# Performance work log

Hardware: AMD Instinct MI355X
Metric: run time of the kernel (lower is better)

Reference implementation:

```python
import jax, jax.numpy as jnp
import numpy as np

B, IN_DIM, D, C = 16384, 1024, 256, 100


def setup_inputs() -> dict:
    key = jax.random.key(0)
    k1, k2, k3, k4 = jax.random.split(key, 4)
    x = jax.random.normal(k1, (B, IN_DIM), dtype=jnp.float32)
    W = jax.random.normal(k2, (IN_DIM, D), dtype=jnp.float32) * (1.0 / np.sqrt(IN_DIM))
    b = jax.random.normal(k3, (D,), dtype=jnp.float32) * 0.01
    P = jax.random.normal(k4, (C, D), dtype=jnp.float32)  # class prototypes [C, D]
    return {"x": x, "W": W, "b": b, "P": P}


def reference(x, W, b, P):
    # Encoder: Z = x @ W + b  -> [B, D]
    Z = x @ W + b
    d = Z.shape[-1]
    # MSE(r, p) = mean((r - p)^2) = (|r|^2 - 2 r.p + |p|^2) / D
    # Computed via expansion to avoid the [B, C, D] broadcast intermediate.
    sq = (
        jnp.sum(Z * Z, axis=-1, keepdims=True)      # [B, 1]
        - 2.0 * (Z @ P.T)                            # [B, C]
        + jnp.sum(P * P, axis=-1)[None, :]           # [1, C]
    )
    return -sq / d  # [B, C]
```

## Files before the change

kernel.cpp:

```cpp
#include <hip/hip_runtime.h>

#define BATCH 16384
#define KDIM  1024
#define DDIM  256
#define CNUM  100
#define CPAD  112
#define RSTR  72

typedef __bf16 bf16x8 __attribute__((ext_vector_type(8)));
typedef float  floatx4 __attribute__((ext_vector_type(4)));

static __device__ __forceinline__ unsigned short f2b(float f) {
    return __builtin_bit_cast(unsigned short, (__bf16)f);
}

__global__ __launch_bounds__(256) void prep(const float* __restrict__ W,
                                            const float* __restrict__ P,
                                            unsigned short* __restrict__ Wt2,
                                            unsigned short* __restrict__ Pbf,
                                            float* __restrict__ pnorm2) {
    __shared__ float T[32][33];
    const int bid = blockIdx.x;
    if (bid < 256) {
        const int k0 = (bid & 31) * 32;
        const int n0 = (bid >> 5) * 32;
        const int j  = threadIdx.x & 31;
        const int i0 = threadIdx.x >> 5;
#pragma unroll
        for (int l = 0; l < 4; ++l) {
            int i = i0 + l * 8;
            T[i][j] = W[(k0 + i) * DDIM + n0 + j];
        }
        __syncthreads();
        if (threadIdx.x < 128) {
            const int l  = threadIdx.x & 63;
            const int fn = threadIdx.x >> 6;
            const int lm = l & 15, lq = l >> 4;
            bf16x8 v;
#pragma unroll
            for (int jj = 0; jj < 8; ++jj)
                v[jj] = (__bf16)T[lq * 8 + jj][fn * 16 + lm];
            const int nblk = (n0 >> 4) + fn;
            const int kblk = k0 >> 5;
            *(bf16x8*)&Wt2[(nblk * 32 + kblk) * 512 + l * 8] = v;
        }
    } else {
        const int wave = threadIdx.x >> 6;
        const int lane = threadIdx.x & 63;
        const int c = (bid - 256) * 4 + wave;
        float s = 0.f;
#pragma unroll
        for (int jj = 0; jj < 4; ++jj) {
            int d = jj * 64 + lane;
            float v = (c < CNUM) ? P[c * DDIM + d] : 0.f;
            Pbf[c * DDIM + d] = f2b(v);
            s += v * v;
        }
#pragma unroll
        for (int m = 1; m < 64; m <<= 1) s += __shfl_xor(s, m, 64);
        if (lane == 0) pnorm2[c] = s;
    }
}

#define CVT8(H, A_, B_)                                                        \
    H[0] = (__bf16)A_[0]; H[1] = (__bf16)A_[1];                                \
    H[2] = (__bf16)A_[2]; H[3] = (__bf16)A_[3];                                \
    H[4] = (__bf16)B_[0]; H[5] = (__bf16)B_[1];                                \
    H[6] = (__bf16)B_[2]; H[7] = (__bf16)B_[3];

#define MFMA_(A_, B_, C_) __builtin_amdgcn_mfma_f32_16x16x32_bf16(A_, B_, C_, 0, 0, 0)

#define GRAN(G, CUR)                                                           \
    {                                                                          \
        const unsigned short* As_c = U16 + (CUR) * 16384 + kh * 8192;          \
        _Pragma("unroll")                                                      \
        for (int kf = 0; kf < 2; ++kf) {                                       \
            const int sw = ((((G) & 1) * 8 + kf * 4 + lq) ^ lm) * 8;           \
            bf16x8 a0 = *(const bf16x8*)&As_c[lm * 128 + sw];                  \
            bf16x8 a1 = *(const bf16x8*)&As_c[(16 + lm) * 128 + sw];           \
            bf16x8 a2 = *(const bf16x8*)&As_c[(32 + lm) * 128 + sw];           \
            bf16x8 a3 = *(const bf16x8*)&As_c[(48 + lm) * 128 + sw];           \
            _Pragma("unroll")                                                  \
            for (int f = 0; f < 4; ++f) {                                      \
                acc[0][f] = MFMA_(a0, b[(G) & 1][kf * 4 + f], acc[0][f]);      \
                acc[1][f] = MFMA_(a1, b[(G) & 1][kf * 4 + f], acc[1][f]);      \
                acc[2][f] = MFMA_(a2, b[(G) & 1][kf * 4 + f], acc[2][f]);      \
                acc[3][f] = MFMA_(a3, b[(G) & 1][kf * 4 + f], acc[3][f]);      \
            }                                                                  \
        }                                                                      \
        if ((G) + 2 < 8) {                                                     \
            _Pragma("unroll")                                                  \
            for (int kf = 0; kf < 2; ++kf)                                     \
                _Pragma("unroll")                                              \
                for (int f = 0; f < 4; ++f)                                    \
                    b[(G) & 1][kf * 4 + f] = *(const bf16x8*)(gB +             \
                        f * 16384 + (((G) + 2) * 2 + kf) * 512);               \
        }                                                                      \
    }

#define PAIRSTEP(T, CUR, NXT)                                                  \
    {                                                                          \
        if ((T) < 3) {                                                         \
            bf16x8 h0, h1, h2, h3;                                             \
            CVT8(h0, p[0], p[1]) CVT8(h1, p[2], p[3])                          \
            CVT8(h2, p[4], p[5]) CVT8(h3, p[6], p[7])                          \
            *(bf16x8*)&U16[(NXT) * 16384 + ldsW0] = h0;                        \
            *(bf16x8*)&U16[(NXT) * 16384 + ldsW1] = h1;                        \
            *(bf16x8*)&U16[(NXT) * 16384 + 8192 + ldsW0] = h2;                 \
            *(bf16x8*)&U16[(NXT) * 16384 + 8192 + ldsW1] = h3;                 \
            if ((T) < 2) {                                                     \
                p[0] = *(const floatx4*)(gA + ((T) + 2) * 128);                \
                p[1] = *(const floatx4*)(gA + ((T) + 2) * 128 + 4);            \
                p[2] = *(const floatx4*)(gA + ((T) + 2) * 128 + 64);           \
                p[3] = *(const floatx4*)(gA + ((T) + 2) * 128 + 68);           \
                p[4] = *(const floatx4*)(gA + 512 + ((T) + 2) * 128);          \
                p[5] = *(const floatx4*)(gA + 512 + ((T) + 2) * 128 + 4);      \
                p[6] = *(const floatx4*)(gA + 512 + ((T) + 2) * 128 + 64);     \
                p[7] = *(const floatx4*)(gA + 512 + ((T) + 2) * 128 + 68);     \
            }                                                                  \
        }                                                                      \
        GRAN(2 * (T), CUR)                                                     \
        GRAN(2 * (T) + 1, CUR)                                                 \
        asm volatile("s_waitcnt lgkmcnt(0)\n\ts_barrier" ::: "memory");        \
    }

__global__ __launch_bounds__(512, 2) void fused_main(
    const float* __restrict__ x, const float* __restrict__ bias,
    const unsigned short* __restrict__ Wt2, const unsigned short* __restrict__ Pbf,
    const float* __restrict__ pnorm2, float* __restrict__ out)
{
    __shared__ __align__(16) float Ubuf[DDIM * RSTR];
    __shared__ float rn2[4][64];
    unsigned short* U16 = (unsigned short*)Ubuf;
    float* Rs = Ubuf;
    unsigned short* Zs = (unsigned short*)Ubuf;

    const int tid  = threadIdx.x;
    const int wave = tid >> 6;
    const int kh   = wave >> 2;
    const int wn   = wave & 3;
    const int lane = tid & 63;
    const int lm   = lane & 15;
    const int lq   = lane >> 4;
    const int r0   = blockIdx.x * 64;

    const int rowA = tid >> 3;
    const int kbA  = tid & 7;
    const float* gA = x + (size_t)(r0 + rowA) * KDIM + kbA * 8;
    const int ldsW0 = rowA * 128 + ((kbA ^ (rowA & 15)) * 8);
    const int ldsW1 = rowA * 128 + (((kbA + 8) ^ (rowA & 15)) * 8);

    const unsigned short* gB = Wt2 + wn * 65536 + kh * 8192 + lane * 8;

    floatx4 acc[4][4];
#pragma unroll
    for (int g = 0; g < 4; ++g)
#pragma unroll
        for (int f = 0; f < 4; ++f) { acc[g][f][0]=0.f; acc[g][f][1]=0.f; acc[g][f][2]=0.f; acc[g][f][3]=0.f; }

    bf16x8  b[2][8];
    floatx4 p[8];

    {
        floatx4 q0 = *(const floatx4*)(gA);
        floatx4 q1 = *(const floatx4*)(gA + 4);
        floatx4 q2 = *(const floatx4*)(gA + 64);
        floatx4 q3 = *(const floatx4*)(gA + 68);
        floatx4 q4 = *(const floatx4*)(gA + 512);
        floatx4 q5 = *(const floatx4*)(gA + 516);
        floatx4 q6 = *(const floatx4*)(gA + 576);
        floatx4 q7 = *(const floatx4*)(gA + 580);
        bf16x8 h0, h1, h2, h3;
        CVT8(h0, q0, q1) CVT8(h1, q2, q3) CVT8(h2, q4, q5) CVT8(h3, q6, q7)
        *(bf16x8*)&U16[ldsW0] = h0;
        *(bf16x8*)&U16[ldsW1] = h1;
        *(bf16x8*)&U16[8192 + ldsW0] = h2;
        *(bf16x8*)&U16[8192 + ldsW1] = h3;
    }
#pragma unroll
    for (int kf = 0; kf < 2; ++kf)
#pragma unroll
        for (int f = 0; f < 4; ++f) {
            b[0][kf * 4 + f] = *(const bf16x8*)(gB + f * 16384 + kf * 512);
            b[1][kf * 4 + f] = *(const bf16x8*)(gB + f * 16384 + (2 + kf) * 512);
        }
    p[0] = *(const floatx4*)(gA + 128);
    p[1] = *(const floatx4*)(gA + 132);
    p[2] = *(const floatx4*)(gA + 192);
    p[3] = *(const floatx4*)(gA + 196);
    p[4] = *(const floatx4*)(gA + 640);
    p[5] = *(const floatx4*)(gA + 644);
    p[6] = *(const floatx4*)(gA + 704);
    p[7] = *(const floatx4*)(gA + 708);
    asm volatile("s_waitcnt lgkmcnt(0)\n\ts_barrier" ::: "memory");

    PAIRSTEP(0, 0, 1)
    PAIRSTEP(1, 1, 0)
    PAIRSTEP(2, 0, 1)
    PAIRSTEP(3, 1, 0)

    if (kh == 1) {
#pragma unroll
        for (int g = 0; g < 4; ++g)
#pragma unroll
            for (int f = 0; f < 4; ++f)
                *(floatx4*)&Rs[(wn * 64 + f * 16 + lm) * RSTR + g * 16 + lq * 4] = acc[g][f];
    }
    __syncthreads();
    if (kh == 0) {
#pragma unroll
        for (int g = 0; g < 4; ++g)
#pragma unroll
            for (int f = 0; f < 4; ++f) {
                floatx4 pp = *(const floatx4*)&Rs[(wn * 64 + f * 16 + lm) * RSTR + g * 16 + lq * 4];
#pragma unroll
                for (int r = 0; r < 4; ++r) acc[g][f][r] += pp[r];
            }
#pragma unroll
        for (int f = 0; f < 4; ++f) {
            float bb = bias[wn * 64 + f * 16 + lm];
#pragma unroll
            for (int g = 0; g < 4; ++g)
#pragma unroll
                for (int r = 0; r < 4; ++r) acc[g][f][r] += bb;
        }
#pragma unroll
        for (int g = 0; g < 4; ++g) {
            float s0 = 0.f, s1 = 0.f, s2 = 0.f, s3 = 0.f;
#pragma unroll
            for (int f = 0; f < 4; ++f) {
                s0 += acc[g][f][0] * acc[g][f][0];
                s1 += acc[g][f][1] * acc[g][f][1];
                s2 += acc[g][f][2] * acc[g][f][2];
                s3 += acc[g][f][3] * acc[g][f][3];
            }
#pragma unroll
            for (int m = 1; m < 16; m <<= 1) {
                s0 += __shfl_xor(s0, m, 64);
                s1 += __shfl_xor(s1, m, 64);
                s2 += __shfl_xor(s2, m, 64);
                s3 += __shfl_xor(s3, m, 64);
            }
            if (lm == 0) {
                int rl = g * 16 + lq * 4;
                rn2[wn][rl + 0] = s0;
                rn2[wn][rl + 1] = s1;
                rn2[wn][rl + 2] = s2;
                rn2[wn][rl + 3] = s3;
            }
        }
    }
    __syncthreads();

    if (kh == 0) {
#pragma unroll
        for (int g = 0; g < 4; ++g)
#pragma unroll
            for (int f = 0; f < 4; ++f) {
                int col = wn * 64 + f * 16 + lm;
#pragma unroll
                for (int r = 0; r < 4; ++r)
                    Zs[(g * 16 + lq * 4 + r) * 264 + col] = f2b(acc[g][f][r]);
            }
    }
    __syncthreads();

    {
        const int ct = wave;
        if (ct < 7) {
            floatx4 acc2[4];
#pragma unroll
            for (int nf = 0; nf < 4; ++nf) { acc2[nf][0]=0.f; acc2[nf][1]=0.f; acc2[nf][2]=0.f; acc2[nf][3]=0.f; }
            const unsigned short* gP = Pbf + (ct * 16 + lm) * DDIM + lq * 8;
#pragma unroll
            for (int ks = 0; ks < 8; ++ks) {
                bf16x8 ap = *(const bf16x8*)(gP + ks * 32);
#pragma unroll
                for (int nf = 0; nf < 4; ++nf) {
                    bf16x8 bz = *(const bf16x8*)&Zs[(nf * 16 + lm) * 264 + ks * 32 + lq * 8];
                    acc2[nf] = __builtin_amdgcn_mfma_f32_16x16x32_bf16(ap, bz, acc2[nf], 0, 0, 0);
                }
            }
            int c0 = ct * 16 + lq * 4;
            if (c0 < CNUM) {
                floatx4 pn = *(const floatx4*)(pnorm2 + c0);
#pragma unroll
                for (int nf = 0; nf < 4; ++nf) {
                    int rl = nf * 16 + lm;
                    float rn = rn2[0][rl] + rn2[1][rl] + rn2[2][rl] + rn2[3][rl];
                    floatx4 o;
#pragma unroll
                    for (int r = 0; r < 4; ++r)
                        o[r] = (2.f * acc2[nf][r] - rn - pn[r]) * (1.f / 256.f);
                    *(floatx4*)&out[(r0 + rl) * CNUM + c0] = o;
                }
            }
        }
    }
}

extern "C" void kernel_launch(void* const* d_in, const int* in_sizes, int n_in,
                              void* d_out, int out_size, void* d_ws, size_t ws_size,
                              hipStream_t stream) {
    const float* x = (const float*)d_in[0];
    const float* W = (const float*)d_in[1];
    const float* b = (const float*)d_in[2];
    const float* P = (const float*)d_in[3];
    float* out = (float*)d_out;

    unsigned short* Wt2 = (unsigned short*)d_ws;
    unsigned short* Pbf = Wt2 + KDIM * DDIM;
    float* pn2 = (float*)(Pbf + CPAD * DDIM);

    prep<<<256 + CPAD / 4, 256, 0, stream>>>(W, P, Wt2, Pbf, pn2);
    fused_main<<<BATCH / 64, 512, 0, stream>>>(x, b, Wt2, Pbf, pn2, out);
}
```

Baseline: 110.9 us.

## Double LDS stage size to halve barriers in x-tile pipeline

After: 110.8 us. Within noise of the previous version (-0.1%).

```diff
diff --git a/kernel.cpp b/kernel.cpp
--- a/kernel.cpp
+++ b/kernel.cpp
@@ -70,16 +70,37 @@
 
 #define MFMA_(A_, B_, C_) __builtin_amdgcn_mfma_f32_16x16x32_bf16(A_, B_, C_, 0, 0, 0)
 
+#define STAGE_LD(PP, Q, T)                                                     \
+    PP[0] = *(const floatx4*)(gA + (Q) * 256 + (T) * 128);                     \
+    PP[1] = *(const floatx4*)(gA + (Q) * 256 + (T) * 128 + 4);                 \
+    PP[2] = *(const floatx4*)(gA + (Q) * 256 + (T) * 128 + 64);                \
+    PP[3] = *(const floatx4*)(gA + (Q) * 256 + (T) * 128 + 68);                \
+    PP[4] = *(const floatx4*)(gA + 512 + (Q) * 256 + (T) * 128);               \
+    PP[5] = *(const floatx4*)(gA + 512 + (Q) * 256 + (T) * 128 + 4);           \
+    PP[6] = *(const floatx4*)(gA + 512 + (Q) * 256 + (T) * 128 + 64);          \
+    PP[7] = *(const floatx4*)(gA + 512 + (Q) * 256 + (T) * 128 + 68);
+
+#define STAGE_WR(PP, BUF, T)                                                   \
+    {                                                                          \
+        bf16x8 h0, h1, h2, h3;                                                 \
+        CVT8(h0, PP[0], PP[1]) CVT8(h1, PP[2], PP[3])                          \
+        CVT8(h2, PP[4], PP[5]) CVT8(h3, PP[6], PP[7])                          \
+        *(bf16x8*)&U16[(BUF) * 32768 + w0 + (T) * 128] = h0;                   \
+        *(bf16x8*)&U16[(BUF) * 32768 + w1 + (T) * 128] = h1;                   \
+        *(bf16x8*)&U16[(BUF) * 32768 + 16384 + w0 + (T) * 128] = h2;           \
+        *(bf16x8*)&U16[(BUF) * 32768 + 16384 + w1 + (T) * 128] = h3;           \
+    }
+
 #define GRAN(G, CUR)                                                           \
     {                                                                          \
-        const unsigned short* As_c = U16 + (CUR) * 16384 + kh * 8192;          \
+        const unsigned short* As_c = U16 + (CUR) * 32768 + kh * 16384;         \
         _Pragma("unroll")                                                      \
         for (int kf = 0; kf < 2; ++kf) {                                       \
-            const int sw = ((((G) & 1) * 8 + kf * 4 + lq) ^ lm) * 8;           \
-            bf16x8 a0 = *(const bf16x8*)&As_c[lm * 128 + sw];                  \
-            bf16x8 a1 = *(const bf16x8*)&As_c[(16 + lm) * 128 + sw];           \
-            bf16x8 a2 = *(const bf16x8*)&As_c[(32 + lm) * 128 + sw];           \
-            bf16x8 a3 = *(const bf16x8*)&As_c[(48 + lm) * 128 + sw];           \
+            const int sw = ((((G) & 3) * 8 + kf * 4 + lq) ^ lm) * 8;           \
+            bf16x8 a0 = *(const bf16x8*)&As_c[lm * 256 + sw];                  \
+            bf16x8 a1 = *(const bf16x8*)&As_c[(16 + lm) * 256 + sw];           \
+            bf16x8 a2 = *(const bf16x8*)&As_c[(32 + lm) * 256 + sw];           \
+            bf16x8 a3 = *(const bf16x8*)&As_c[(48 + lm) * 256 + sw];           \
             _Pragma("unroll")                                                  \
             for (int f = 0; f < 4; ++f) {                                      \
                 acc[0][f] = MFMA_(a0, b[(G) & 1][kf * 4 + f], acc[0][f]);      \
@@ -98,38 +119,14 @@
         }                                                                      \
     }
 
-#define PAIRSTEP(T, CUR, NXT)                                                  \
-    {                                                                          \
-        if ((T) < 3) {                                                         \
-            bf16x8 h0, h1, h2, h3;                                             \
-            CVT8(h0, p[0], p[1]) CVT8(h1, p[2], p[3])                          \
-            CVT8(h2, p[4], p[5]) CVT8(h3, p[6], p[7])                          \
-            *(bf16x8*)&U16[(NXT) * 16384 + ldsW0] = h0;                        \
-            *(bf16x8*)&U16[(NXT) * 16384 + ldsW1] = h1;                        \
-            *(bf16x8*)&U16[(NXT) * 16384 + 8192 + ldsW0] = h2;                 \
-            *(bf16x8*)&U16[(NXT) * 16384 + 8192 + ldsW1] = h3;                 \
-            if ((T) < 2) {                                                     \
-                p[0] = *(const floatx4*)(gA + ((T) + 2) * 128);                \
-                p[1] = *(const floatx4*)(gA + ((T) + 2) * 128 + 4);            \
-                p[2] = *(const floatx4*)(gA + ((T) + 2) * 128 + 64);           \
-                p[3] = *(const floatx4*)(gA + ((T) + 2) * 128 + 68);           \
-                p[4] = *(const floatx4*)(gA + 512 + ((T) + 2) * 128);          \
-                p[5] = *(const floatx4*)(gA + 512 + ((T) + 2) * 128 + 4);      \
-                p[6] = *(const floatx4*)(gA + 512 + ((T) + 2) * 128 + 64);     \
-                p[7] = *(const floatx4*)(gA + 512 + ((T) + 2) * 128 + 68);     \
-            }                                                                  \
-        }                                                                      \
-        GRAN(2 * (T), CUR)                                                     \
-        GRAN(2 * (T) + 1, CUR)                                                 \
-        asm volatile("s_waitcnt lgkmcnt(0)\n\ts_barrier" ::: "memory");        \
-    }
+#define BARRIER asm volatile("s_waitcnt lgkmcnt(0)\n\ts_barrier" ::: "memory");
 
 __global__ __launch_bounds__(512, 2) void fused_main(
     const float* __restrict__ x, const float* __restrict__ bias,
     const unsigned short* __restrict__ Wt2, const unsigned short* __restrict__ Pbf,
     const float* __restrict__ pnorm2, float* __restrict__ out)
 {
-    __shared__ __align__(16) float Ubuf[DDIM * RSTR];
+    __shared__ __align__(16) float Ubuf[32768];
     __shared__ float rn2[4][64];
     unsigned short* U16 = (unsigned short*)Ubuf;
     float* Rs = Ubuf;
@@ -147,8 +144,9 @@
     const int rowA = tid >> 3;
     const int kbA  = tid & 7;
     const float* gA = x + (size_t)(r0 + rowA) * KDIM + kbA * 8;
-    const int ldsW0 = rowA * 128 + ((kbA ^ (rowA & 15)) * 8);
-    const int ldsW1 = rowA * 128 + (((kbA + 8) ^ (rowA & 15)) * 8);
+    const int m15 = rowA & 15;
+    const int w0 = rowA * 256 + ((kbA ^ m15) * 8);
+    const int w1 = rowA * 256 + (((kbA + 8) ^ m15) * 8);
 
     const unsigned short* gB = Wt2 + wn * 65536 + kh * 8192 + lane * 8;
 
@@ -159,24 +157,10 @@
         for (int f = 0; f < 4; ++f) { acc[g][f][0]=0.f; acc[g][f][1]=0.f; acc[g][f][2]=0.f; acc[g][f][3]=0.f; }
 
     bf16x8  b[2][8];
-    floatx4 p[8];
-
-    {
-        floatx4 q0 = *(const floatx4*)(gA);
-        floatx4 q1 = *(const floatx4*)(gA + 4);
-        floatx4 q2 = *(const floatx4*)(gA + 64);
-        floatx4 q3 = *(const floatx4*)(gA + 68);
-        floatx4 q4 = *(const floatx4*)(gA + 512);
-        floatx4 q5 = *(const floatx4*)(gA + 516);
-        floatx4 q6 = *(const floatx4*)(gA + 576);
-        floatx4 q7 = *(const floatx4*)(gA + 580);
-        bf16x8 h0, h1, h2, h3;
-        CVT8(h0, q0, q1) CVT8(h1, q2, q3) CVT8(h2, q4, q5) CVT8(h3, q6, q7)
-        *(bf16x8*)&U16[ldsW0] = h0;
-        *(bf16x8*)&U16[ldsW1] = h1;
-        *(bf16x8*)&U16[8192 + ldsW0] = h2;
-        *(bf16x8*)&U16[8192 + ldsW1] = h3;
-    }
+    floatx4 pA[8], pB[8];
+
+    STAGE_LD(pA, 0, 0)
+    STAGE_LD(pB, 0, 1)
 #pragma unroll
     for (int kf = 0; kf < 2; ++kf)
 #pragma unroll
@@ -184,20 +168,25 @@
             b[0][kf * 4 + f] = *(const bf16x8*)(gB + f * 16384 + kf * 512);
             b[1][kf * 4 + f] = *(const bf16x8*)(gB + f * 16384 + (2 + kf) * 512);
         }
-    p[0] = *(const floatx4*)(gA + 128);
-    p[1] = *(const floatx4*)(gA + 132);
-    p[2] = *(const floatx4*)(gA + 192);
-    p[3] = *(const floatx4*)(gA + 196);
-    p[4] = *(const floatx4*)(gA + 640);
-    p[5] = *(const floatx4*)(gA + 644);
-    p[6] = *(const floatx4*)(gA + 704);
-    p[7] = *(const floatx4*)(gA + 708);
-    asm volatile("s_waitcnt lgkmcnt(0)\n\ts_barrier" ::: "memory");
-
-    PAIRSTEP(0, 0, 1)
-    PAIRSTEP(1, 1, 0)
-    PAIRSTEP(2, 0, 1)
-    PAIRSTEP(3, 1, 0)
+    STAGE_WR(pA, 0, 0)
+    STAGE_LD(pA, 1, 0)
+    STAGE_WR(pB, 0, 1)
+    BARRIER
+
+    STAGE_WR(pA, 1, 0)
+    STAGE_LD(pB, 1, 1)
+    GRAN(0, 0)
+    GRAN(1, 0)
+    STAGE_WR(pB, 1, 1)
+    GRAN(2, 0)
+    GRAN(3, 0)
+    BARRIER
+
+    GRAN(4, 1)
+    GRAN(5, 1)
+    GRAN(6, 1)
+    GRAN(7, 1)
+    BARRIER
 
     if (kh == 1) {
 #pragma unroll
```
